# Kernel tuning notes

Hardware: AMD Instinct MI355X
Metric: run time of the kernel (lower is better)

## Reference

```python
import jax, jax.numpy as jnp
import numpy as np

S = 4096      # packed sequence length
DIM = 1024    # model dim
H = 8         # num heads
HD = 64       # per-branch head dim (head_dim // 2 in the module)
LAMBDA_INIT = 0.8 - 0.6 * float(np.exp(-0.3 * 0.0))  # depth=0 -> 0.2
EPS = 1e-5


def setup_inputs() -> dict:
    key = jax.random.key(0)
    ks = jax.random.split(key, 10)
    P = 2 * H * HD  # = 1024
    return {
        "x": jax.random.normal(ks[0], (S, DIM), jnp.float32),
        "mask": jnp.ones((1, 1, S, S), jnp.bool_),
        "Wq": jax.random.normal(ks[1], (DIM, P), jnp.float32) * 0.02,
        "Wk": jax.random.normal(ks[2], (DIM, P), jnp.float32) * 0.02,
        "Wv": jax.random.normal(ks[3], (DIM, P), jnp.float32) * 0.02,
        "Wo": jax.random.normal(ks[4], (P, DIM), jnp.float32) * 0.02,
        "lambda_q1": jax.random.normal(ks[5], (HD,), jnp.float32) * 0.1,
        "lambda_k1": jax.random.normal(ks[6], (HD,), jnp.float32) * 0.1,
        "lambda_q2": jax.random.normal(ks[7], (HD,), jnp.float32) * 0.1,
        "lambda_k2": jax.random.normal(ks[8], (HD,), jnp.float32) * 0.1,
        "subln_weight": jnp.ones((2 * HD,), jnp.float32),
    }


def reference(x, mask, Wq, Wk, Wv, Wo, lambda_q1, lambda_k1, lambda_q2,
              lambda_k2, subln_weight):
    # projections: (S, 2H, HD) split into branch index along a new axis
    xq = (x @ Wq).reshape(S, H, 2, HD)   # [2*H] view -> (H,2) contiguous split
    xk = (x @ Wk).reshape(S, H, 2, HD)
    xv = (x @ Wv).reshape(S, H, 2 * HD)
    q1, q2 = xq[:, :, 0], xq[:, :, 1]    # (S,H,HD)
    k1, k2 = xk[:, :, 0], xk[:, :, 1]

    scale = 1.0 / jnp.sqrt(jnp.float32(HD))
    bias = jnp.where(mask[0, 0], 0.0, -jnp.inf)  # (S,S) additive mask

    def sdpa(q, k):
        # q,k: (S,H,HD); xv: (S,H,2HD)
        scores = jnp.einsum('shd,thd->hst', q, k) * scale + bias  # (H,S,S)
        p = jax.nn.softmax(scores, axis=-1)
        return jnp.einsum('hst,thd->shd', p, xv)                  # (S,H,2HD)

    attn1 = sdpa(q1, k1)
    attn2 = sdpa(q2, k2)

    lam1 = jnp.exp(jnp.sum(lambda_q1 * lambda_k1))
    lam2 = jnp.exp(jnp.sum(lambda_q2 * lambda_k2))
    lambda_full = lam1 - lam2 + LAMBDA_INIT

    attn = attn1 - lambda_full * attn2                            # (S,H,2HD)
    # RMSNorm over last dim (2*HD) with learnable weight
    attn = attn * jax.lax.rsqrt(jnp.mean(attn * attn, axis=-1, keepdims=True) + EPS)
    attn = attn * subln_weight
    attn = attn * (1.0 - LAMBDA_INIT)
    return attn.reshape(S, H * 2 * HD) @ Wo                       # (S, DIM)
```

## Files before the change

### kernel.cpp

```cpp
#include <hip/hip_runtime.h>
#include <hip/hip_bf16.h>
#include <type_traits>
#include <utility>


using bf16 = __hip_bfloat16;

static constexpr int SQ = 4096;
static constexpr int DM = 1024;
static constexpr float LAMB_INIT = 0.2f;

typedef float  f32x4    __attribute__((ext_vector_type(4)));
typedef short  s16x4    __attribute__((ext_vector_type(4)));
typedef short  bf16x8_i __attribute__((ext_vector_type(8)));
typedef __bf16 bf16x8_b __attribute__((ext_vector_type(8)));

template<typename T, typename = void> struct mfma_ok : std::false_type {};
template<typename T> struct mfma_ok<T, std::void_t<decltype(
    __builtin_amdgcn_mfma_f32_16x16x32_bf16(std::declval<T>(), std::declval<T>(),
                                            std::declval<f32x4>(), 0, 0, 0))>>
    : std::true_type {};
using abfrag = std::conditional_t<mfma_ok<bf16x8_b>::value, bf16x8_b, bf16x8_i>;

__device__ __forceinline__ f32x4 mfma16(abfrag a, abfrag b, f32x4 c) {
    return __builtin_amdgcn_mfma_f32_16x16x32_bf16(a, b, c, 0, 0, 0);
}
__device__ __forceinline__ abfrag ldfrag(const bf16* p) {
    return *reinterpret_cast<const abfrag*>(p);
}
__device__ __forceinline__ short bf2s(bf16 b) {
    short s; __builtin_memcpy(&s, &b, 2); return s;
}
__device__ __forceinline__ float fexp2(float x) {
#if __has_builtin(__builtin_amdgcn_exp2f)
    return __builtin_amdgcn_exp2f(x);
#else
    return exp2f(x);
#endif
}
__device__ __forceinline__ void gld_lds16(const bf16* g, bf16* l) {
    __builtin_amdgcn_global_load_lds((__attribute__((address_space(1))) void*)g,
                                     (__attribute__((address_space(3))) void*)l,
                                     16, 0, 0);
}


__global__ __launch_bounds__(256) void convert_x(const float* __restrict__ in,
                                                 bf16* __restrict__ outp)
{
    const size_t i = ((size_t)blockIdx.x * 256 + threadIdx.x) * 4;
    const f32x4 v = *reinterpret_cast<const f32x4*>(in + i);
    s16x4 o;
#pragma unroll
    for (int j = 0; j < 4; ++j) o[j] = bf2s(__float2bfloat16(v[j]));
    *reinterpret_cast<s16x4*>(outp + i) = o;
}

__global__ __launch_bounds__(256) void transpose_w(
    const float* __restrict__ Wq, const float* __restrict__ Wk,
    const float* __restrict__ Wv, const float* __restrict__ Wo,
    bf16* __restrict__ Wqt, bf16* __restrict__ Wkt,
    bf16* __restrict__ Wvt, bf16* __restrict__ Wot)
{
    const int z = blockIdx.z;
    const float* src = (z == 0) ? Wq : (z == 1) ? Wk : (z == 2) ? Wv : Wo;
    bf16* dst        = (z == 0) ? Wqt : (z == 1) ? Wkt : (z == 2) ? Wvt : Wot;
    __shared__ float tbuf[32][33];
    const int k0 = blockIdx.x * 32, n0 = blockIdx.y * 32;
    const int c = threadIdx.x & 31, r0 = threadIdx.x >> 5;
#pragma unroll
    for (int i = 0; i < 4; ++i)
        tbuf[r0 + i * 8][c] = src[(size_t)(k0 + r0 + i * 8) * 1024 + n0 + c];
    __syncthreads();
#pragma unroll
    for (int i = 0; i < 4; ++i)
        dst[(size_t)(n0 + r0 + i * 8) * 1024 + k0 + c] =
            __float2bfloat16(tbuf[c][r0 + i * 8]);
}

__global__ __launch_bounds__(256) void transpose_v(const bf16* __restrict__ V,
                                                   bf16* __restrict__ Vt)
{
    __shared__ bf16 tbuf[32][33];
    const int s0 = blockIdx.x * 32, n0 = blockIdx.y * 32;
    const int c = threadIdx.x & 31, r0 = threadIdx.x >> 5;
#pragma unroll
    for (int i = 0; i < 4; ++i)
        tbuf[r0 + i * 8][c] = V[(size_t)(s0 + r0 + i * 8) * 1024 + n0 + c];
    __syncthreads();
#pragma unroll
    for (int i = 0; i < 4; ++i)
        Vt[(size_t)(n0 + r0 + i * 8) * 4096 + s0 + c] = tbuf[c][r0 + i * 8];
}

__global__ void lambda_kernel(const float* lq1, const float* lk1,
                              const float* lq2, const float* lk2, float* outp)
{
    const int lane = threadIdx.x;
    float a = lq1[lane] * lk1[lane];
    float b = lq2[lane] * lk2[lane];
#pragma unroll
    for (int m = 1; m < 64; m <<= 1) {
        a += __shfl_xor(a, m, 64);
        b += __shfl_xor(b, m, 64);
    }
    if (lane == 0) outp[0] = __expf(a) - __expf(b) + LAMB_INIT;
}


template<bool BF16OUT>
__device__ __forceinline__ void gemm_core(const bf16* __restrict__ A,
                                          const bf16* __restrict__ Bt,
                                          void* __restrict__ Cout,
                                          int m0, int n0, int ldc)
{
    __shared__ __align__(16) bf16 As[128 * 32];
    __shared__ __align__(16) bf16 Bs[128 * 32];
    const int tid  = threadIdx.x;
    const int wid  = tid >> 6;
    const int lane = tid & 63;
    const int l15  = lane & 15;
    const int l4   = lane >> 4;
    const int wr   = wid >> 1;
    const int wc   = wid & 1;

    const f32x4 zero4 = {0.f, 0.f, 0.f, 0.f};
    f32x4 acc[4][4];
#pragma unroll
    for (int i = 0; i < 4; ++i)
#pragma unroll
        for (int j = 0; j < 4; ++j) acc[i][j] = zero4;

    for (int kt = 0; kt < 1024; kt += 32) {
        __syncthreads();
#pragma unroll
        for (int it = 0; it < 2; ++it) {
            const int flat = it * 256 + tid;
            const int row  = flat >> 2;
            const int c16  = flat & 3;
            const int ldst = (it * 256 + wid * 64) * 8;
            gld_lds16(&A [(size_t)(m0 + row) * 1024 + kt + c16 * 8], &As[ldst]);
            gld_lds16(&Bt[(size_t)(n0 + row) * 1024 + kt + c16 * 8], &Bs[ldst]);
        }
        __syncthreads();
        abfrag a[4], b[4];
#pragma unroll
        for (int mi = 0; mi < 4; ++mi)
            a[mi] = ldfrag(&As[(wr * 64 + mi * 16 + l15) * 32 + l4 * 8]);
#pragma unroll
        for (int ni = 0; ni < 4; ++ni)
            b[ni] = ldfrag(&Bs[(wc * 64 + ni * 16 + l15) * 32 + l4 * 8]);
#pragma unroll
        for (int mi = 0; mi < 4; ++mi)
#pragma unroll
            for (int ni = 0; ni < 4; ++ni)
                acc[mi][ni] = mfma16(a[mi], b[ni], acc[mi][ni]);
    }

#pragma unroll
    for (int mi = 0; mi < 4; ++mi)
#pragma unroll
        for (int ni = 0; ni < 4; ++ni)
#pragma unroll
            for (int r = 0; r < 4; ++r) {
                const int row = m0 + wr * 64 + mi * 16 + l4 * 4 + r;
                const int col = n0 + wc * 64 + ni * 16 + l15;
                if constexpr (BF16OUT)
                    ((bf16*)Cout)[(size_t)row * ldc + col] = __float2bfloat16(acc[mi][ni][r]);
                else
                    ((float*)Cout)[(size_t)row * ldc + col] = acc[mi][ni][r];
            }
}

__global__ __launch_bounds__(256, 2) void gemm_qkv(
    const bf16* __restrict__ xbf,
    const bf16* __restrict__ Wqt, const bf16* __restrict__ Wkt,
    const bf16* __restrict__ Wvt,
    bf16* __restrict__ Qo, bf16* __restrict__ Ko, bf16* __restrict__ Vo)
{
    const int which = blockIdx.y >> 3;
    const bf16* Bt = (which == 0) ? Wqt : (which == 1) ? Wkt : Wvt;
    bf16* Cp       = (which == 0) ? Qo  : (which == 1) ? Ko  : Vo;
    gemm_core<true>(xbf, Bt, Cp, blockIdx.x * 128, (blockIdx.y & 7) * 128, 1024);
}

__global__ __launch_bounds__(256, 2) void gemm_out(
    const bf16* __restrict__ Amat, const bf16* __restrict__ Wot,
    float* __restrict__ out)
{
    gemm_core<false>(Amat, Wot, out, blockIdx.x * 128, blockIdx.y * 128, 1024);
}


__global__ __launch_bounds__(256, 2) void flash_diff(
    const bf16* __restrict__ Qm, const bf16* __restrict__ Km,
    const bf16* __restrict__ Vtm, const float* __restrict__ lam_ptr,
    const float* __restrict__ subln, bf16* __restrict__ Amat)
{
    const int bid  = blockIdx.x;
    const int h    = bid & 7;
    const int qt   = bid >> 3;
    const int tid  = threadIdx.x;
    const int wid  = tid >> 6;
    const int lane = tid & 63;
    const int l15  = lane & 15;
    const int l4   = lane >> 4;
    const int qbase = qt * 64 + wid * 16;
    const int swz   = (l15 & 7) << 4;

    constexpr float KSC  = 0.18033688f;
    constexpr float INVK = 1.0f / KSC;
    constexpr float THR  = 8.0f;

    __shared__ __align__(16) bf16 KB[2][64 * 128];
    __shared__ __align__(16) bf16 VB[2][128 * 64];

    abfrag qf[2][2];
#pragma unroll
    for (int c = 0; c < 2; ++c)
#pragma unroll
        for (int kc = 0; kc < 2; ++kc)
            qf[c][kc] = ldfrag(&Qm[(size_t)(qbase + l15) * DM +
                                   h * 128 + c * 64 + kc * 32 + l4 * 8]);

    auto stage = [&](int buf, int kvb) {
#pragma unroll
        for (int it = 0; it < 4; ++it) {
            {
                const int slot = it * 256 + tid;
                const int row  = slot >> 4;
                const int scb  = ((slot & 15) << 4) ^ ((row & 7) << 4);
                gld_lds16(&Km[(size_t)(kvb + row) * DM + h * 128 + (scb >> 1)],
                          &KB[buf][(it * 256 + wid * 64) * 8]);
            }
            {
                const int slot = it * 256 + tid;
                const int row  = slot >> 3;
                const int scb  = ((slot & 7) << 4) ^ ((row & 7) << 4);
                gld_lds16(&Vtm[(size_t)(h * 128 + row) * SQ + kvb + (scb >> 1)],
                          &VB[buf][(it * 256 + wid * 64) * 8]);
            }
        }
    };

    const f32x4 zero4 = {0.f, 0.f, 0.f, 0.f};
    f32x4 o_[2][8];
#pragma unroll
    for (int c = 0; c < 2; ++c)
#pragma unroll
        for (int vt = 0; vt < 8; ++vt) o_[c][vt] = zero4;
    float m_loc[2]  = {-1e30f, -1e30f};
    float l_part[2] = {0.f, 0.f};
    float thresh[2] = {-1e28f, -1e28f};

    stage(0, 0);
    __syncthreads();

    int cur = 0;
    constexpr int NT = SQ / 64;
#pragma unroll 1
    for (int t = 0; t < NT; ++t) {
        if (t + 1 < NT) stage(cur ^ 1, (t + 1) * 64);

        const char* kb = (const char*)KB[cur];
        const char* vb = (const char*)VB[cur];

        abfrag pa[2][2];
#pragma unroll
        for (int c = 0; c < 2; ++c) {
            f32x4 sc[4];
#pragma unroll
            for (int j = 0; j < 4; ++j) {
                const char* kr = kb + (j * 16 + l15) * 256;
                const abfrag k0 = *(const abfrag*)(kr + ((c * 128 + l4 * 16) ^ swz));
                const abfrag k1 = *(const abfrag*)(kr + ((c * 128 + 64 + l4 * 16) ^ swz));
                f32x4 z = zero4;
                z = mfma16(k0, qf[c][0], z);
                sc[j] = mfma16(k1, qf[c][1], z);
            }
            float lmx = fmaxf(fmaxf(sc[0][0], sc[0][1]), fmaxf(sc[0][2], sc[0][3]));
#pragma unroll
            for (int j = 1; j < 4; ++j)
                lmx = fmaxf(lmx, fmaxf(fmaxf(sc[j][0], sc[j][1]),
                                       fmaxf(sc[j][2], sc[j][3])));
            if (__any(lmx > thresh[c])) {
                float mx = lmx;
                mx = fmaxf(mx, __shfl_xor(mx, 16, 64));
                mx = fmaxf(mx, __shfl_xor(mx, 32, 64));
                const float nm    = fmaxf(m_loc[c], mx * KSC);
                const float alpha = fexp2(m_loc[c] - nm);
                m_loc[c]  = nm;
                thresh[c] = (nm + THR) * INVK;
                l_part[c] *= alpha;
#pragma unroll
                for (int r = 0; r < 4; ++r) {
                    const float alr = __shfl(alpha, l4 * 4 + r, 64);
#pragma unroll
                    for (int vt = 0; vt < 8; ++vt) o_[c][vt][r] *= alr;
                }
            }
            const float mcur = m_loc[c];
            float rs = 0.f;
            f32x4 pe[4];
#pragma unroll
            for (int j = 0; j < 4; ++j)
#pragma unroll
                for (int r = 0; r < 4; ++r) {
                    const float pv = fexp2(__builtin_fmaf(sc[j][r], KSC, -mcur));
                    pe[j][r] = pv;
                    rs += pv;
                }
            l_part[c] += rs;
            union { abfrag f; short s[8]; } u0, u1;
#pragma unroll
            for (int r = 0; r < 4; ++r) {
                u0.s[r]     = bf2s(__float2bfloat16(pe[0][r]));
                u0.s[4 + r] = bf2s(__float2bfloat16(pe[1][r]));
                u1.s[r]     = bf2s(__float2bfloat16(pe[2][r]));
                u1.s[4 + r] = bf2s(__float2bfloat16(pe[3][r]));
            }
            pa[c][0] = u0.f;
            pa[c][1] = u1.f;
        }

        __builtin_amdgcn_s_setprio(1);
#pragma unroll
        for (int vt = 0; vt < 8; ++vt) {
            const char* vr = vb + (vt * 16 + l15) * 128;
#pragma unroll
            for (int ch = 0; ch < 2; ++ch) {
                union { abfrag f; s16x4 hh[2]; } vv;
                vv.hh[0] = *(const s16x4*)(vr + ((ch * 64 + l4 * 8) ^ swz));
                vv.hh[1] = *(const s16x4*)(vr + ((ch * 64 + 32 + l4 * 8) ^ swz));
                o_[0][vt] = mfma16(pa[0][ch], vv.f, o_[0][vt]);
                o_[1][vt] = mfma16(pa[1][ch], vv.f, o_[1][vt]);
            }
        }
        __builtin_amdgcn_s_setprio(0);

        __syncthreads();
        cur ^= 1;
    }

#pragma unroll
    for (int c = 0; c < 2; ++c) {
        l_part[c] += __shfl_xor(l_part[c], 16, 64);
        l_part[c] += __shfl_xor(l_part[c], 32, 64);
    }

    const float lam = lam_ptr[0];
    float il1[4], il2[4];
#pragma unroll
    for (int r = 0; r < 4; ++r) {
        il1[r] = 1.f / __shfl(l_part[0], l4 * 4 + r, 64);
        il2[r] = lam / __shfl(l_part[1], l4 * 4 + r, 64);
    }
#pragma unroll
    for (int r = 0; r < 4; ++r) {
        float comb[8];
        float ss = 0.f;
#pragma unroll
        for (int vt = 0; vt < 8; ++vt) {
            const float v = o_[0][vt][r] * il1[r] - o_[1][vt][r] * il2[r];
            comb[vt] = v;
            ss += v * v;
        }
        ss += __shfl_xor(ss, 1, 64);
        ss += __shfl_xor(ss, 2, 64);
        ss += __shfl_xor(ss, 4, 64);
        ss += __shfl_xor(ss, 8, 64);
        const float rinv = rsqrtf(ss * (1.f / 128.f) + 1e-5f);
        const int row = qbase + l4 * 4 + r;
#pragma unroll
        for (int vt = 0; vt < 8; ++vt) {
            const float outv = comb[vt] * rinv * subln[vt * 16 + l15] * 0.8f;
            Amat[(size_t)row * DM + h * 128 + vt * 16 + l15] = __float2bfloat16(outv);
        }
    }
}


extern "C" void kernel_launch(void* const* d_in, const int* in_sizes, int n_in,
                              void* d_out, int out_size, void* d_ws, size_t ws_size,
                              hipStream_t stream)
{
    (void)in_sizes; (void)n_in; (void)out_size; (void)ws_size;
    const float* x    = (const float*)d_in[0];
    const float* Wq   = (const float*)d_in[2];
    const float* Wk   = (const float*)d_in[3];
    const float* Wv   = (const float*)d_in[4];
    const float* Wo   = (const float*)d_in[5];
    const float* lq1  = (const float*)d_in[6];
    const float* lk1  = (const float*)d_in[7];
    const float* lq2  = (const float*)d_in[8];
    const float* lk2  = (const float*)d_in[9];
    const float* subw = (const float*)d_in[10];

    char* ws = (char*)d_ws;
    size_t off = 0;
    auto take = [&](size_t n) { void* p = ws + off; off += (n + 255) & ~(size_t)255; return p; };
    bf16* xbf = (bf16*)take((size_t)SQ * DM * 2);
    bf16* Wqt = (bf16*)take((size_t)DM * DM * 2);
    bf16* Wkt = (bf16*)take((size_t)DM * DM * 2);
    bf16* Wvt = (bf16*)take((size_t)DM * DM * 2);
    bf16* Wot = (bf16*)take((size_t)DM * DM * 2);
    bf16* Qb  = (bf16*)take((size_t)SQ * DM * 2);
    bf16* Kb  = (bf16*)take((size_t)SQ * DM * 2);
    bf16* Vb  = (bf16*)take((size_t)SQ * DM * 2);
    bf16* Vtb = (bf16*)take((size_t)SQ * DM * 2);
    bf16* Am  = (bf16*)take((size_t)SQ * DM * 2);
    float* lamp = (float*)take(256);

    convert_x   <<<dim3(SQ * DM / 1024), dim3(256), 0, stream>>>(x, xbf);
    transpose_w <<<dim3(32, 32, 4),      dim3(256), 0, stream>>>(Wq, Wk, Wv, Wo, Wqt, Wkt, Wvt, Wot);
    lambda_kernel<<<dim3(1),             dim3(64),  0, stream>>>(lq1, lk1, lq2, lk2, lamp);
    gemm_qkv    <<<dim3(32, 24),         dim3(256), 0, stream>>>(xbf, Wqt, Wkt, Wvt, Qb, Kb, Vb);
    transpose_v <<<dim3(128, 32),        dim3(256), 0, stream>>>(Vb, Vtb);
    flash_diff  <<<dim3(512),            dim3(256), 0, stream>>>(Qb, Kb, Vtb, lamp, subw, Am);
    gemm_out    <<<dim3(32, 8),          dim3(256), 0, stream>>>(Am, Wot, (float*)d_out);
}
```

Before: 196.6 us.

## Fold softmax scale into Wq, bias MFMA accumulator with running max, sum via MFMA

```diff
diff --git a/kernel.cpp b/kernel.cpp
--- a/kernel.cpp
+++ b/kernel.cpp
@@ -9,6 +9,7 @@
 static constexpr int SQ = 4096;
 static constexpr int DM = 1024;
 static constexpr float LAMB_INIT = 0.2f;
+static constexpr float KSC = 0.18033688011112043f;
 
 typedef float  f32x4    __attribute__((ext_vector_type(4)));
 typedef short  s16x4    __attribute__((ext_vector_type(4)));
@@ -65,6 +66,7 @@
     const int z = blockIdx.z;
     const float* src = (z == 0) ? Wq : (z == 1) ? Wk : (z == 2) ? Wv : Wo;
     bf16* dst        = (z == 0) ? Wqt : (z == 1) ? Wkt : (z == 2) ? Wvt : Wot;
+    const float scale = (z == 0) ? KSC : 1.0f;
     __shared__ float tbuf[32][33];
     const int k0 = blockIdx.x * 32, n0 = blockIdx.y * 32;
     const int c = threadIdx.x & 31, r0 = threadIdx.x >> 5;
@@ -75,7 +77,7 @@
 #pragma unroll
     for (int i = 0; i < 4; ++i)
         dst[(size_t)(n0 + r0 + i * 8) * 1024 + k0 + c] =
-            __float2bfloat16(tbuf[c][r0 + i * 8]);
+            __float2bfloat16(tbuf[c][r0 + i * 8] * scale);
 }
 
 __global__ __launch_bounds__(256) void transpose_v(const bf16* __restrict__ V,
@@ -208,9 +210,7 @@
     const int qbase = qt * 64 + wid * 16;
     const int swz   = (l15 & 7) << 4;
 
-    constexpr float KSC  = 0.18033688f;
-    constexpr float INVK = 1.0f / KSC;
-    constexpr float THR  = 8.0f;
+    constexpr float THR = 8.0f;
 
     __shared__ __align__(16) bf16 KB[2][64 * 128];
     __shared__ __align__(16) bf16 VB[2][128 * 64];
@@ -223,23 +223,30 @@
             qf[c][kc] = ldfrag(&Qm[(size_t)(qbase + l15) * DM +
                                    h * 128 + c * 64 + kc * 32 + l4 * 8]);
 
-    auto stage = [&](int buf, int kvb) {
+    union { abfrag f; short s[8]; } uon;
+#pragma unroll
+    for (int i = 0; i < 8; ++i) uon.s[i] = (short)0x3F80;
+    const abfrag ones = uon.f;
+
+    const bf16* kap[4];
+    const bf16* vap[4];
+#pragma unroll
+    for (int it = 0; it < 4; ++it) {
+        const int slot = it * 256 + tid;
+        const int krow = slot >> 4;
+        const int kscb = ((slot & 15) << 4) ^ ((krow & 7) << 4);
+        kap[it] = &Km[(size_t)krow * DM + h * 128 + (kscb >> 1)];
+        const int vrow = slot >> 3;
+        const int vscb = ((slot & 7) << 4) ^ ((vrow & 7) << 4);
+        vap[it] = &Vtm[(size_t)(h * 128 + vrow) * SQ + (vscb >> 1)];
+    }
+    auto stage = [&](int buf) {
 #pragma unroll
         for (int it = 0; it < 4; ++it) {
-            {
-                const int slot = it * 256 + tid;
-                const int row  = slot >> 4;
-                const int scb  = ((slot & 15) << 4) ^ ((row & 7) << 4);
-                gld_lds16(&Km[(size_t)(kvb + row) * DM + h * 128 + (scb >> 1)],
-                          &KB[buf][(it * 256 + wid * 64) * 8]);
-            }
-            {
-                const int slot = it * 256 + tid;
-                const int row  = slot >> 3;
-                const int scb  = ((slot & 7) << 4) ^ ((row & 7) << 4);
-                gld_lds16(&Vtm[(size_t)(h * 128 + row) * SQ + kvb + (scb >> 1)],
-                          &VB[buf][(it * 256 + wid * 64) * 8]);
-            }
+            gld_lds16(kap[it], &KB[buf][(it * 256 + wid * 64) * 8]);
+            gld_lds16(vap[it], &VB[buf][(it * 256 + wid * 64) * 8]);
+            kap[it] += 64 * DM;
+            vap[it] += 64;
         }
     };
 
@@ -249,18 +256,17 @@
     for (int c = 0; c < 2; ++c)
 #pragma unroll
         for (int vt = 0; vt < 8; ++vt) o_[c][vt] = zero4;
-    float m_loc[2]  = {-1e30f, -1e30f};
-    float l_part[2] = {0.f, 0.f};
-    float thresh[2] = {-1e28f, -1e28f};
-
-    stage(0, 0);
+    f32x4 lacc[2] = {zero4, zero4};
+    float m_loc[2] = {0.f, 0.f};
+
+    stage(0);
     __syncthreads();
 
     int cur = 0;
     constexpr int NT = SQ / 64;
 #pragma unroll 1
     for (int t = 0; t < NT; ++t) {
-        if (t + 1 < NT) stage(cur ^ 1, (t + 1) * 64);
+        if (t + 1 < NT) stage(cur ^ 1);
 
         const char* kb = (const char*)KB[cur];
         const char* vb = (const char*)VB[cur];
@@ -268,14 +274,15 @@
         abfrag pa[2][2];
 #pragma unroll
         for (int c = 0; c < 2; ++c) {
+            const float mc = m_loc[c];
+            const f32x4 binit = {-mc, -mc, -mc, -mc};
             f32x4 sc[4];
 #pragma unroll
             for (int j = 0; j < 4; ++j) {
                 const char* kr = kb + (j * 16 + l15) * 256;
                 const abfrag k0 = *(const abfrag*)(kr + ((c * 128 + l4 * 16) ^ swz));
                 const abfrag k1 = *(const abfrag*)(kr + ((c * 128 + 64 + l4 * 16) ^ swz));
-                f32x4 z = zero4;
-                z = mfma16(k0, qf[c][0], z);
+                f32x4 z = mfma16(k0, qf[c][0], binit);
                 sc[j] = mfma16(k1, qf[c][1], z);
             }
             float lmx = fmaxf(fmaxf(sc[0][0], sc[0][1]), fmaxf(sc[0][2], sc[0][3]));
@@ -283,34 +290,29 @@
             for (int j = 1; j < 4; ++j)
                 lmx = fmaxf(lmx, fmaxf(fmaxf(sc[j][0], sc[j][1]),
                                        fmaxf(sc[j][2], sc[j][3])));
-            if (__any(lmx > thresh[c])) {
+            if (__any(lmx > THR)) {
                 float mx = lmx;
                 mx = fmaxf(mx, __shfl_xor(mx, 16, 64));
                 mx = fmaxf(mx, __shfl_xor(mx, 32, 64));
-                const float nm    = fmaxf(m_loc[c], mx * KSC);
-                const float alpha = fexp2(m_loc[c] - nm);
-                m_loc[c]  = nm;
-                thresh[c] = (nm + THR) * INVK;
-                l_part[c] *= alpha;
+                const float alpha = fexp2(-mx);
+                m_loc[c] += mx;
 #pragma unroll
                 for (int r = 0; r < 4; ++r) {
                     const float alr = __shfl(alpha, l4 * 4 + r, 64);
 #pragma unroll
                     for (int vt = 0; vt < 8; ++vt) o_[c][vt][r] *= alr;
+                    lacc[c][r] *= alr;
                 }
+#pragma unroll
+                for (int j = 0; j < 4; ++j)
+#pragma unroll
+                    for (int r = 0; r < 4; ++r) sc[j][r] -= mx;
             }
-            const float mcur = m_loc[c];
-            float rs = 0.f;
             f32x4 pe[4];
 #pragma unroll
             for (int j = 0; j < 4; ++j)
 #pragma unroll
-                for (int r = 0; r < 4; ++r) {
-                    const float pv = fexp2(__builtin_fmaf(sc[j][r], KSC, -mcur));
-                    pe[j][r] = pv;
-                    rs += pv;
-                }
-            l_part[c] += rs;
+                for (int r = 0; r < 4; ++r) pe[j][r] = fexp2(sc[j][r]);
             union { abfrag f; short s[8]; } u0, u1;
 #pragma unroll
             for (int r = 0; r < 4; ++r) {
@@ -324,6 +326,10 @@
         }
 
         __builtin_amdgcn_s_setprio(1);
+        lacc[0] = mfma16(pa[0][0], ones, lacc[0]);
+        lacc[0] = mfma16(pa[0][1], ones, lacc[0]);
+        lacc[1] = mfma16(pa[1][0], ones, lacc[1]);
+        lacc[1] = mfma16(pa[1][1], ones, lacc[1]);
 #pragma unroll
         for (int vt = 0; vt < 8; ++vt) {
             const char* vr = vb + (vt * 16 + l15) * 128;
@@ -342,18 +348,12 @@
         cur ^= 1;
     }
 
-#pragma unroll
-    for (int c = 0; c < 2; ++c) {
-        l_part[c] += __shfl_xor(l_part[c], 16, 64);
-        l_part[c] += __shfl_xor(l_part[c], 32, 64);
-    }
-
     const float lam = lam_ptr[0];
     float il1[4], il2[4];
 #pragma unroll
     for (int r = 0; r < 4; ++r) {
-        il1[r] = 1.f / __shfl(l_part[0], l4 * 4 + r, 64);
-        il2[r] = lam / __shfl(l_part[1], l4 * 4 + r, 64);
+        il1[r] = 1.f / lacc[0][r];
+        il2[r] = lam / lacc[1][r];
     }
 #pragma unroll
     for (int r = 0; r < 4; ++r) {
```

Result: no change. 194.9 us (-0.9%).
